# Kernel optimization log

Measured on AMD Instinct MI355X. Metric: run time of the kernel, lower is better.

Reference implementation:

```python
import jax, jax.numpy as jnp
import numpy as np

B, N, D, H = 2, 2048, 1024, 16
DH = D // H
MASK_VALUE = -1e7


def setup_inputs() -> dict:
    key = jax.random.key(0)
    ks = jax.random.split(key, 8)
    scale = 0.02
    return {
        "queries": jax.random.normal(ks[0], (B, N, D), dtype=jnp.float32),
        "keys": jax.random.normal(ks[1], (B, N, D), dtype=jnp.float32),
        "values": jax.random.normal(ks[2], (B, N, D), dtype=jnp.float32),
        "valid_len": jax.random.randint(ks[3], (B * H,), 1, N + 1, dtype=jnp.int32),
        "Wq": jax.random.normal(ks[4], (D, D), dtype=jnp.float32) * scale,
        "Wk": jax.random.normal(ks[5], (D, D), dtype=jnp.float32) * scale,
        "Wv": jax.random.normal(ks[6], (D, D), dtype=jnp.float32) * scale,
        "Wo": jax.random.normal(ks[7], (D, D), dtype=jnp.float32) * scale,
    }


def reference(queries, keys, values, valid_len, Wq, Wk, Wv, Wo):
    b, n, d = queries.shape
    h, dh = H, d // H

    def split_heads(x):  # (b, n, d) -> (b, h, n, dh)
        return x.reshape(b, n, h, dh).transpose(0, 2, 1, 3)

    q = split_heads(queries @ Wq)
    k = split_heads(keys @ Wk)
    v = split_heads(values @ Wv)

    # (b, h, nq, nk) full score tensor, as in the original naive bmm path
    scores = jnp.einsum("bhqd,bhkd->bhqk", q, k) / jnp.sqrt(jnp.float32(dh))

    # valid_len is 1-D of length b*h; repeat_interleave over queries means the
    # mask depends only on the key index: keep k < valid_len[bh]
    vl = valid_len.reshape(b, h, 1, 1)
    keep = jnp.arange(n)[None, None, None, :] < vl  # (b, h, 1, nk)
    scores = jnp.where(keep, scores, MASK_VALUE)

    attn = jax.nn.softmax(scores, axis=-1)
    heads = jnp.einsum("bhqk,bhkd->bhqd", attn, v)  # (b, h, n, dh)
    out = heads.transpose(0, 2, 1, 3).reshape(b, n, d) @ Wo
    return out
```

## Files before the change

### kernel.cpp

```cpp
#include <hip/hip_runtime.h>

#define B_ 2
#define N_ 2048
#define D_ 1024
#define H_ 16
#define DH_ 64
#define NITEMS 1024

typedef _Float16 half8 __attribute__((ext_vector_type(8)));
typedef _Float16 half4 __attribute__((ext_vector_type(4)));
typedef float f32x4 __attribute__((ext_vector_type(4)));

__device__ __forceinline__ void gl2lds16(const _Float16* g, _Float16* l) {
  __builtin_amdgcn_global_load_lds(
      (const __attribute__((address_space(1))) void*)g,
      (__attribute__((address_space(3))) void*)l, 16, 0, 0);
}

__global__ __launch_bounds__(256) void convert_x_kernel(
    const float* __restrict__ q, const float* __restrict__ k,
    const float* __restrict__ v, _Float16* __restrict__ dst) {
  const float* s = (blockIdx.y == 0) ? q : (blockIdx.y == 1) ? k : v;
  _Float16* d = dst + (size_t)blockIdx.y * ((size_t)B_ * N_ * D_);
  size_t idx = ((size_t)blockIdx.x * 256 + threadIdx.x) * 8;
  float4 a = *(const float4*)(s + idx);
  float4 b = *(const float4*)(s + idx + 4);
  half8 h;
  h[0] = (_Float16)a.x; h[1] = (_Float16)a.y; h[2] = (_Float16)a.z; h[3] = (_Float16)a.w;
  h[4] = (_Float16)b.x; h[5] = (_Float16)b.y; h[6] = (_Float16)b.z; h[7] = (_Float16)b.w;
  *(half8*)(d + idx) = h;
}

__global__ __launch_bounds__(256) void convert_w_kernel(
    const float* __restrict__ Wq, const float* __restrict__ Wk,
    const float* __restrict__ Wv, const float* __restrict__ Wo,
    _Float16* __restrict__ WtAll) {
  const float* W = (blockIdx.z == 0) ? Wq : (blockIdx.z == 1) ? Wk
                  : (blockIdx.z == 2) ? Wv : Wo;
  _Float16* Wt = WtAll + (size_t)blockIdx.z * D_ * D_;
  __shared__ float tile[64][65];
  int k0 = blockIdx.y * 64, n0 = blockIdx.x * 64;
  int tr = threadIdx.x >> 4, tc = threadIdx.x & 15;
#pragma unroll
  for (int i = 0; i < 4; ++i) {
    int r = tr + i * 16;
    float4 va = *(const float4*)(W + (size_t)(k0 + r) * D_ + n0 + tc * 4);
    tile[r][tc * 4 + 0] = va.x; tile[r][tc * 4 + 1] = va.y;
    tile[r][tc * 4 + 2] = va.z; tile[r][tc * 4 + 3] = va.w;
  }
  __syncthreads();
#pragma unroll
  for (int i = 0; i < 4; ++i) {
    int r = tr + i * 16;
    half4 hv;
    hv[0] = (_Float16)tile[tc * 4 + 0][r];
    hv[1] = (_Float16)tile[tc * 4 + 1][r];
    hv[2] = (_Float16)tile[tc * 4 + 2][r];
    hv[3] = (_Float16)tile[tc * 4 + 3][r];
    *(half4*)(Wt + (size_t)(n0 + r) * D_ + k0 + tc * 4) = hv;
  }
}

template <int NT, int MODE>
__global__ __launch_bounds__(256) void gemm_f16_kernel(
    const _Float16* __restrict__ Aall, const _Float16* __restrict__ Btall,
    _Float16* __restrict__ ChAll, float* __restrict__ Cf32) {
  constexpr int BN = NT * 32;
  constexpr int K = D_;
  __shared__ __attribute__((aligned(16))) _Float16 As[2][128 * 32];
  __shared__ __attribute__((aligned(16))) _Float16 Bs[2][BN * 32];
  const int z = blockIdx.z;
  const _Float16* A  = Aall  + (size_t)z * ((size_t)B_ * N_ * D_);
  const _Float16* Bt = Btall + (size_t)z * ((size_t)D_ * D_);
  _Float16* Chead = ChAll + (size_t)z * ((size_t)B_ * N_ * D_);

  const int tid = threadIdx.x;
  const int m0 = blockIdx.y * 128, n0 = blockIdx.x * BN;
  const int lane = tid & 63, w = tid >> 6;
  const int quad = lane >> 4, l15 = lane & 15;
  const int wm = (w >> 1) * 64, wn = (w & 1) * (BN / 2);
  const int sr = tid >> 2, sc4 = tid & 3;
  f32x4 acc[4][NT] = {};

  auto stage = [&](int kt, int buf) {
#pragma unroll
    for (int p = 0; p < 2; ++p) {
      int row = sr + p * 64;
      int gl = sc4 ^ ((row >> 1) & 3);
      gl2lds16(A + (size_t)(m0 + row) * K + kt + gl * 8,
               &As[buf][(row * 4 + sc4) * 8]);
    }
#pragma unroll
    for (int p = 0; p < NT / 2; ++p) {
      int row = sr + p * 64;
      int gl = sc4 ^ ((row >> 1) & 3);
      gl2lds16(Bt + (size_t)(n0 + row) * K + kt + gl * 8,
               &Bs[buf][(row * 4 + sc4) * 8]);
    }
  };

  stage(0, 0);
  __syncthreads();

  for (int kt = 0; kt < K / 32; ++kt) {
    const int cur = kt & 1;
    if (kt + 1 < K / 32) stage((kt + 1) * 32, 1 - cur);
    half8 af[4], bf[NT];
#pragma unroll
    for (int mt = 0; mt < 4; ++mt) {
      int row = wm + mt * 16 + l15;
      af[mt] = *(const half8*)&As[cur][(row * 4 + (quad ^ ((row >> 1) & 3))) * 8];
    }
#pragma unroll
    for (int nt = 0; nt < NT; ++nt) {
      int row = wn + nt * 16 + l15;
      bf[nt] = *(const half8*)&Bs[cur][(row * 4 + (quad ^ ((row >> 1) & 3))) * 8];
    }
#pragma unroll
    for (int mt = 0; mt < 4; ++mt)
#pragma unroll
      for (int nt = 0; nt < NT; ++nt)
        acc[mt][nt] = __builtin_amdgcn_mfma_f32_16x16x32_f16(
            af[mt], bf[nt], acc[mt][nt], 0, 0, 0);
    __syncthreads();
  }

#pragma unroll
  for (int mt = 0; mt < 4; ++mt) {
    int mrow = m0 + wm + mt * 16 + quad * 4;
#pragma unroll
    for (int nt = 0; nt < NT; ++nt) {
      int jcol = n0 + wn + nt * 16 + l15;
#pragma unroll
      for (int r = 0; r < 4; ++r) {
        float val = acc[mt][nt][r];
        int m = mrow + r;
        if (MODE == 0) {
          int b = m >> 11, n = m & (N_ - 1);
          int h = jcol >> 6, dh = jcol & (DH_ - 1);
          Chead[((((size_t)(b * H_ + h)) * N_ + n) * DH_) + dh] = (_Float16)val;
        } else {
          Cf32[(size_t)m * D_ + jcol] = val;
        }
      }
    }
  }
}

__global__ __launch_bounds__(256) void transpose_v_kernel(
    const _Float16* __restrict__ Vh, _Float16* __restrict__ VtG) {
  __shared__ float Ls[64][65];
  int bh = blockIdx.y, k0 = blockIdx.x * 64;
  int tid = threadIdx.x;
  const _Float16* src = Vh + (size_t)bh * N_ * DH_;
#pragma unroll
  for (int p = 0; p < 2; ++p) {
    int c = p * 256 + tid, row = c >> 3, pg = c & 7;
    half8 hv = *(const half8*)(src + (size_t)(k0 + row) * DH_ + pg * 8);
#pragma unroll
    for (int u = 0; u < 8; ++u) Ls[row][pg * 8 + u] = (float)hv[u];
  }
  __syncthreads();
  _Float16* dst = VtG + (size_t)bh * N_ * DH_;
#pragma unroll
  for (int p = 0; p < 2; ++p) {
    int c = p * 256 + tid, dh = c >> 3, pg = c & 7;
    half8 hv;
#pragma unroll
    for (int u = 0; u < 8; ++u) hv[u] = (_Float16)Ls[pg * 8 + u][dh];
    *(half8*)(dst + (size_t)dh * N_ + k0 + pg * 8) = hv;
  }
}

__global__ void sort_heads_kernel(const int* __restrict__ vlen,
                                  int* __restrict__ order) {
  int i = threadIdx.x;
  if (i < B_ * H_) {
    int vi = vlen[i], rank = 0;
    for (int j = 0; j < B_ * H_; ++j) {
      int vj = vlen[j];
      if (vj > vi || (vj == vi && j < i)) ++rank;
    }
    order[rank] = i;
  }
}

__global__ __launch_bounds__(256, 4) void attn_kernel(
    const _Float16* __restrict__ Qh, const _Float16* __restrict__ Kh,
    const _Float16* __restrict__ VtG, const int* __restrict__ vlen,
    _Float16* __restrict__ Hd, const int* __restrict__ order) {
  __shared__ __attribute__((aligned(16))) _Float16 Ks[2][64 * 64];
  __shared__ __attribute__((aligned(16))) _Float16 Vt[2][64 * 64];
  const int tid = threadIdx.x, lane = tid & 63, w = tid >> 6;
  const int quad = lane >> 4, l15 = lane & 15;
  const int sw  = (quad ^ (l15 & 7)) * 8;
  const int sw2 = ((quad + 4) ^ (l15 & 7)) * 8;
  const float sc2 = 0.125f * 1.44269504088896f;
  const half4 ones = {(_Float16)1, (_Float16)1, (_Float16)1, (_Float16)1};

#pragma unroll 1
  for (int half_ = 0; half_ < 2; ++half_) {
    const int item = half_ ? (NITEMS - 1 - (int)blockIdx.x) : (int)blockIdx.x;
    const int bh = order[item >> 5];
    const int q0 = (item & 31) * 64;
    const int b = bh >> 4, h = bh & (H_ - 1);
    const int vl = vlen[bh];
    const int KT = (vl + 63) >> 6;
    const _Float16* Qb = Qh  + (size_t)bh * N_ * DH_;
    const _Float16* Kb = Kh  + (size_t)bh * N_ * DH_;
    const _Float16* Vb = VtG + (size_t)bh * N_ * DH_;

    const half8 qb0 = *(const half8*)(Qb + (size_t)(q0 + w * 16 + l15) * DH_ + quad * 8);
    const half8 qb1 = *(const half8*)(Qb + (size_t)(q0 + w * 16 + l15) * DH_ + 32 + quad * 8);

    half8 kpre[2], vpre[2];
    auto prefetch = [&](int k0k) {
#pragma unroll
      for (int p = 0; p < 2; ++p) {
        int c = p * 256 + tid;
        int row = c >> 3, pg = c & 7;
        kpre[p] = *(const half8*)(Kb + (size_t)(k0k + row) * DH_ + (pg ^ (row & 7)) * 8);
        vpre[p] = *(const half8*)(Vb + (size_t)row * N_ + k0k + pg * 8);
      }
    };
    auto commit = [&](int buf) {
#pragma unroll
      for (int p = 0; p < 2; ++p) {
        int c = p * 256 + tid;
        int row = c >> 3, pg = c & 7;
        *(half8*)&Ks[buf][c * 8] = kpre[p];
        int j0 = (pg * 2) ^ (row & 15), j1 = (pg * 2 + 1) ^ (row & 15);
        half4 lo = {vpre[p][0], vpre[p][1], vpre[p][2], vpre[p][3]};
        half4 hi = {vpre[p][4], vpre[p][5], vpre[p][6], vpre[p][7]};
        *(half4*)&Vt[buf][row * 64 + j0 * 4] = lo;
        *(half4*)&Vt[buf][row * 64 + j1 * 4] = hi;
      }
    };

    if (half_) __syncthreads();
    prefetch(0);
    commit(0);
    if (KT > 1) prefetch(64);
    __syncthreads();

    f32x4 Oacc[4] = {};
    f32x4 lacc = {};

    for (int kt = 0; kt < KT; ++kt) {
      const int cur = kt & 1;
      if (kt + 1 < KT) commit(1 - cur);
      if (kt + 2 < KT) prefetch((kt + 2) * 64);

      f32x4 s[4];
#pragma unroll
      for (int nt = 0; nt < 4; ++nt) {
        int r = nt * 16 + l15;
        half8 ka0 = *(const half8*)&Ks[cur][r * 64 + sw];
        half8 ka1 = *(const half8*)&Ks[cur][r * 64 + sw2];
        f32x4 c = {};
        c = __builtin_amdgcn_mfma_f32_16x16x32_f16(ka0, qb0, c, 0, 0, 0);
        c = __builtin_amdgcn_mfma_f32_16x16x32_f16(ka1, qb1, c, 0, 0, 0);
        s[nt] = c;
      }
      const int k0k = kt * 64;
      half4 pf[4];
      if (k0k + 64 <= vl) {
#pragma unroll
        for (int nt = 0; nt < 4; ++nt)
#pragma unroll
          for (int r = 0; r < 4; ++r)
            pf[nt][r] = (_Float16)exp2f(s[nt][r] * sc2);
      } else {
#pragma unroll
        for (int nt = 0; nt < 4; ++nt) {
          int keyb = k0k + nt * 16 + quad * 4;
#pragma unroll
          for (int r = 0; r < 4; ++r) {
            float p = exp2f(s[nt][r] * sc2);
            pf[nt][r] = (keyb + r < vl) ? (_Float16)p : (_Float16)0.f;
          }
        }
      }
#pragma unroll
      for (int nt = 0; nt < 4; ++nt) {
        lacc = __builtin_amdgcn_mfma_f32_16x16x16f16(ones, pf[nt], lacc, 0, 0, 0);
#pragma unroll
        for (int dt = 0; dt < 4; ++dt) {
          int dh = dt * 16 + l15;
          half4 va = *(const half4*)&Vt[cur][dh * 64 + (((nt * 4 + quad) ^ l15) << 2)];
          Oacc[dt] = __builtin_amdgcn_mfma_f32_16x16x16f16(va, pf[nt], Oacc[dt], 0, 0, 0);
        }
      }
      __syncthreads();
    }

    float inv_l = 1.0f / lacc[0];
    int q = q0 + w * 16 + l15;
    _Float16* out = Hd + ((size_t)(b * N_ + q)) * D_ + h * DH_;
#pragma unroll
    for (int dt = 0; dt < 4; ++dt) {
      half4 o;
#pragma unroll
      for (int r = 0; r < 4; ++r) o[r] = (_Float16)(Oacc[dt][r] * inv_l);
      *(half4*)(out + dt * 16 + quad * 4) = o;
    }
  }
}

extern "C" void kernel_launch(void* const* d_in, const int* in_sizes, int n_in,
                              void* d_out, int out_size, void* d_ws, size_t ws_size,
                              hipStream_t stream) {
  const float* q  = (const float*)d_in[0];
  const float* k  = (const float*)d_in[1];
  const float* v  = (const float*)d_in[2];
  const int*   vl = (const int*)d_in[3];
  const float* Wq = (const float*)d_in[4];
  const float* Wk = (const float*)d_in[5];
  const float* Wv = (const float*)d_in[6];
  const float* Wo = (const float*)d_in[7];

  const size_t XSZ = (size_t)B_ * N_ * D_;
  const size_t WSZ = (size_t)D_ * D_;
  _Float16* ws = (_Float16*)d_ws;
  _Float16* Xf = ws;
  _Float16* Wt = Xf + 3 * XSZ;
  _Float16* Qh = Wt + 4 * WSZ;
  _Float16* Hd = Qh + 3 * XSZ;
  int* order = (int*)(Hd + XSZ);
  _Float16* VtG = Xf;

  convert_x_kernel<<<dim3(2048, 3), 256, 0, stream>>>(q, k, v, Xf);
  convert_w_kernel<<<dim3(16, 16, 4), 256, 0, stream>>>(Wq, Wk, Wv, Wo, Wt);

  gemm_f16_kernel<4, 0><<<dim3(D_ / 128, 32, 3), 256, 0, stream>>>(
      Xf, Wt, Qh, nullptr);

  transpose_v_kernel<<<dim3(N_ / 64, B_ * H_), 256, 0, stream>>>(
      Qh + 2 * XSZ, VtG);
  sort_heads_kernel<<<1, 64, 0, stream>>>(vl, order);

  attn_kernel<<<dim3(512), 256, 0, stream>>>(
      Qh, Qh + XSZ, VtG, vl, Hd, order);

  gemm_f16_kernel<2, 1><<<dim3(D_ / 64, 32, 1), 256, 0, stream>>>(
      Hd, Wt + 3 * WSZ, nullptr, (float*)d_out);
}
```

Measured before the change: 240.8 us.

## Merge prep kernels, single-buffer GEMM staging, one attention tile per block

Folds the X conversion, weight transpose-convert and head-sort kernels into one prep kernel launch, which removes two launches. The GEMM drops its double-buffered LDS staging for a single buffer with a sync before and after each k-step. This halves LDS use but stops loads from overlapping with MFMA work. The attention kernel now launches 1024 blocks, each handling one query tile, instead of 512 blocks that each paired a long and a short tile. Load balance across heads of different lengths now rests on the hardware scheduler and the sorted order.

```diff
diff --git a/kernel.cpp b/kernel.cpp
--- a/kernel.cpp
+++ b/kernel.cpp
@@ -17,49 +17,65 @@
       (__attribute__((address_space(3))) void*)l, 16, 0, 0);
 }
 
-__global__ __launch_bounds__(256) void convert_x_kernel(
+__global__ __launch_bounds__(256) void prep_kernel(
     const float* __restrict__ q, const float* __restrict__ k,
-    const float* __restrict__ v, _Float16* __restrict__ dst) {
-  const float* s = (blockIdx.y == 0) ? q : (blockIdx.y == 1) ? k : v;
-  _Float16* d = dst + (size_t)blockIdx.y * ((size_t)B_ * N_ * D_);
-  size_t idx = ((size_t)blockIdx.x * 256 + threadIdx.x) * 8;
-  float4 a = *(const float4*)(s + idx);
-  float4 b = *(const float4*)(s + idx + 4);
-  half8 h;
-  h[0] = (_Float16)a.x; h[1] = (_Float16)a.y; h[2] = (_Float16)a.z; h[3] = (_Float16)a.w;
-  h[4] = (_Float16)b.x; h[5] = (_Float16)b.y; h[6] = (_Float16)b.z; h[7] = (_Float16)b.w;
-  *(half8*)(d + idx) = h;
-}
-
-__global__ __launch_bounds__(256) void convert_w_kernel(
-    const float* __restrict__ Wq, const float* __restrict__ Wk,
-    const float* __restrict__ Wv, const float* __restrict__ Wo,
-    _Float16* __restrict__ WtAll) {
-  const float* W = (blockIdx.z == 0) ? Wq : (blockIdx.z == 1) ? Wk
-                  : (blockIdx.z == 2) ? Wv : Wo;
-  _Float16* Wt = WtAll + (size_t)blockIdx.z * D_ * D_;
+    const float* __restrict__ v, const float* __restrict__ Wq,
+    const float* __restrict__ Wk, const float* __restrict__ Wv,
+    const float* __restrict__ Wo, const int* __restrict__ vlen,
+    _Float16* __restrict__ Xf, _Float16* __restrict__ WtAll,
+    int* __restrict__ order) {
   __shared__ float tile[64][65];
-  int k0 = blockIdx.y * 64, n0 = blockIdx.x * 64;
-  int tr = threadIdx.x >> 4, tc = threadIdx.x & 15;
-#pragma unroll
-  for (int i = 0; i < 4; ++i) {
-    int r = tr + i * 16;
-    float4 va = *(const float4*)(W + (size_t)(k0 + r) * D_ + n0 + tc * 4);
-    tile[r][tc * 4 + 0] = va.x; tile[r][tc * 4 + 1] = va.y;
-    tile[r][tc * 4 + 2] = va.z; tile[r][tc * 4 + 3] = va.w;
-  }
-  __syncthreads();
-#pragma unroll
-  for (int i = 0; i < 4; ++i) {
-    int r = tr + i * 16;
-    half4 hv;
-    hv[0] = (_Float16)tile[tc * 4 + 0][r];
-    hv[1] = (_Float16)tile[tc * 4 + 1][r];
-    hv[2] = (_Float16)tile[tc * 4 + 2][r];
-    hv[3] = (_Float16)tile[tc * 4 + 3][r];
-    *(half4*)(Wt + (size_t)(n0 + r) * D_ + k0 + tc * 4) = hv;
-  }
-}
+  const int bid = blockIdx.x;
+  if (bid < 6144) {
+    int y = bid >> 11, x = bid & 2047;
+    const float* s = (y == 0) ? q : (y == 1) ? k : v;
+    _Float16* d = Xf + (size_t)y * ((size_t)B_ * N_ * D_);
+    size_t idx = ((size_t)x * 256 + threadIdx.x) * 8;
+    float4 a = *(const float4*)(s + idx);
+    float4 b = *(const float4*)(s + idx + 4);
+    half8 h;
+    h[0] = (_Float16)a.x; h[1] = (_Float16)a.y; h[2] = (_Float16)a.z; h[3] = (_Float16)a.w;
+    h[4] = (_Float16)b.x; h[5] = (_Float16)b.y; h[6] = (_Float16)b.z; h[7] = (_Float16)b.w;
+    *(half8*)(d + idx) = h;
+  } else if (bid < 6144 + 1024) {
+    int idx = bid - 6144;
+    int z = idx >> 8, rem = idx & 255, gy = rem >> 4, gx = rem & 15;
+    const float* W = (z == 0) ? Wq : (z == 1) ? Wk : (z == 2) ? Wv : Wo;
+    _Float16* Wt = WtAll + (size_t)z * D_ * D_;
+    int k0 = gy * 64, n0 = gx * 64;
+    int tr = threadIdx.x >> 4, tc = threadIdx.x & 15;
+#pragma unroll
+    for (int i = 0; i < 4; ++i) {
+      int r = tr + i * 16;
+      float4 va = *(const float4*)(W + (size_t)(k0 + r) * D_ + n0 + tc * 4);
+      tile[r][tc * 4 + 0] = va.x; tile[r][tc * 4 + 1] = va.y;
+      tile[r][tc * 4 + 2] = va.z; tile[r][tc * 4 + 3] = va.w;
+    }
+    __syncthreads();
+#pragma unroll
+    for (int i = 0; i < 4; ++i) {
+      int r = tr + i * 16;
+      half4 hv;
+      hv[0] = (_Float16)tile[tc * 4 + 0][r];
+      hv[1] = (_Float16)tile[tc * 4 + 1][r];
+      hv[2] = (_Float16)tile[tc * 4 + 2][r];
+      hv[3] = (_Float16)tile[tc * 4 + 3][r];
+      *(half4*)(Wt + (size_t)(n0 + r) * D_ + k0 + tc * 4) = hv;
+    }
+  } else {
+    int i = threadIdx.x;
+    if (i < B_ * H_) {
+      int vi = vlen[i], rank = 0;
+      for (int j = 0; j < B_ * H_; ++j) {
+        int vj = vlen[j];
+        if (vj > vi || (vj == vi && j < i)) ++rank;
+      }
+      order[rank] = i;
+    }
+  }
+}
+
+#define BK 32
 
 template <int NT, int MODE>
 __global__ __launch_bounds__(256) void gemm_f16_kernel(
@@ -67,8 +83,8 @@
     _Float16* __restrict__ ChAll, float* __restrict__ Cf32) {
   constexpr int BN = NT * 32;
   constexpr int K = D_;
-  __shared__ __attribute__((aligned(16))) _Float16 As[2][128 * 32];
-  __shared__ __attribute__((aligned(16))) _Float16 Bs[2][BN * 32];
+  __shared__ __attribute__((aligned(16))) _Float16 As[128 * BK];
+  __shared__ __attribute__((aligned(16))) _Float16 Bs[BN * BK];
   const int z = blockIdx.z;
   const _Float16* A  = Aall  + (size_t)z * ((size_t)B_ * N_ * D_);
   const _Float16* Bt = Btall + (size_t)z * ((size_t)D_ * D_);
@@ -79,50 +95,39 @@
   const int lane = tid & 63, w = tid >> 6;
   const int quad = lane >> 4, l15 = lane & 15;
   const int wm = (w >> 1) * 64, wn = (w & 1) * (BN / 2);
-  const int sr = tid >> 2, sc4 = tid & 3;
+  const int swz = (quad ^ ((l15 >> 1) & 3)) * 8;
   f32x4 acc[4][NT] = {};
 
-  auto stage = [&](int kt, int buf) {
+  for (int kt = 0; kt < K; kt += BK) {
+    if (kt) __syncthreads();
 #pragma unroll
     for (int p = 0; p < 2; ++p) {
-      int row = sr + p * 64;
-      int gl = sc4 ^ ((row >> 1) & 3);
-      gl2lds16(A + (size_t)(m0 + row) * K + kt + gl * 8,
-               &As[buf][(row * 4 + sc4) * 8]);
+      int c = p * 256 + tid;
+      int row = c >> 2, pg = c & 3;
+      int gl = pg ^ ((row >> 1) & 3);
+      gl2lds16(A + (size_t)(m0 + row) * K + kt + gl * 8, &As[c * 8]);
     }
 #pragma unroll
     for (int p = 0; p < NT / 2; ++p) {
-      int row = sr + p * 64;
-      int gl = sc4 ^ ((row >> 1) & 3);
-      gl2lds16(Bt + (size_t)(n0 + row) * K + kt + gl * 8,
-               &Bs[buf][(row * 4 + sc4) * 8]);
-    }
-  };
-
-  stage(0, 0);
-  __syncthreads();
-
-  for (int kt = 0; kt < K / 32; ++kt) {
-    const int cur = kt & 1;
-    if (kt + 1 < K / 32) stage((kt + 1) * 32, 1 - cur);
+      int c = p * 256 + tid;
+      int row = c >> 2, pg = c & 3;
+      int gl = pg ^ ((row >> 1) & 3);
+      gl2lds16(Bt + (size_t)(n0 + row) * K + kt + gl * 8, &Bs[c * 8]);
+    }
+    __syncthreads();
     half8 af[4], bf[NT];
 #pragma unroll
-    for (int mt = 0; mt < 4; ++mt) {
-      int row = wm + mt * 16 + l15;
-      af[mt] = *(const half8*)&As[cur][(row * 4 + (quad ^ ((row >> 1) & 3))) * 8];
-    }
-#pragma unroll
-    for (int nt = 0; nt < NT; ++nt) {
-      int row = wn + nt * 16 + l15;
-      bf[nt] = *(const half8*)&Bs[cur][(row * 4 + (quad ^ ((row >> 1) & 3))) * 8];
-    }
+    for (int mt = 0; mt < 4; ++mt)
+      af[mt] = *(const half8*)&As[(wm + mt * 16 + l15) * 32 + swz];
+#pragma unroll
+    for (int nt = 0; nt < NT; ++nt)
+      bf[nt] = *(const half8*)&Bs[(wn + nt * 16 + l15) * 32 + swz];
 #pragma unroll
     for (int mt = 0; mt < 4; ++mt)
 #pragma unroll
       for (int nt = 0; nt < NT; ++nt)
         acc[mt][nt] = __builtin_amdgcn_mfma_f32_16x16x32_f16(
             af[mt], bf[nt], acc[mt][nt], 0, 0, 0);
-    __syncthreads();
   }
 
 #pragma unroll
@@ -169,19 +174,6 @@
 #pragma unroll
     for (int u = 0; u < 8; ++u) hv[u] = (_Float16)Ls[pg * 8 + u][dh];
     *(half8*)(dst + (size_t)dh * N_ + k0 + pg * 8) = hv;
-  }
-}
-
-__global__ void sort_heads_kernel(const int* __restrict__ vlen,
-                                  int* __restrict__ order) {
-  int i = threadIdx.x;
-  if (i < B_ * H_) {
-    int vi = vlen[i], rank = 0;
-    for (int j = 0; j < B_ * H_; ++j) {
-      int vj = vlen[j];
-      if (vj > vi || (vj == vi && j < i)) ++rank;
-    }
-    order[rank] = i;
   }
 }
 
@@ -198,112 +190,108 @@
   const float sc2 = 0.125f * 1.44269504088896f;
   const half4 ones = {(_Float16)1, (_Float16)1, (_Float16)1, (_Float16)1};
 
-#pragma unroll 1
-  for (int half_ = 0; half_ < 2; ++half_) {
-    const int item = half_ ? (NITEMS - 1 - (int)blockIdx.x) : (int)blockIdx.x;
-    const int bh = order[item >> 5];
-    const int q0 = (item & 31) * 64;
-    const int b = bh >> 4, h = bh & (H_ - 1);
-    const int vl = vlen[bh];
-    const int KT = (vl + 63) >> 6;
-    const _Float16* Qb = Qh  + (size_t)bh * N_ * DH_;
-    const _Float16* Kb = Kh  + (size_t)bh * N_ * DH_;
-    const _Float16* Vb = VtG + (size_t)bh * N_ * DH_;
-
-    const half8 qb0 = *(const half8*)(Qb + (size_t)(q0 + w * 16 + l15) * DH_ + quad * 8);
-    const half8 qb1 = *(const half8*)(Qb + (size_t)(q0 + w * 16 + l15) * DH_ + 32 + quad * 8);
-
-    half8 kpre[2], vpre[2];
-    auto prefetch = [&](int k0k) {
-#pragma unroll
-      for (int p = 0; p < 2; ++p) {
-        int c = p * 256 + tid;
-        int row = c >> 3, pg = c & 7;
-        kpre[p] = *(const half8*)(Kb + (size_t)(k0k + row) * DH_ + (pg ^ (row & 7)) * 8);
-        vpre[p] = *(const half8*)(Vb + (size_t)row * N_ + k0k + pg * 8);
-      }
-    };
-    auto commit = [&](int buf) {
-#pragma unroll
-      for (int p = 0; p < 2; ++p) {
-        int c = p * 256 + tid;
-        int row = c >> 3, pg = c & 7;
-        *(half8*)&Ks[buf][c * 8] = kpre[p];
-        int j0 = (pg * 2) ^ (row & 15), j1 = (pg * 2 + 1) ^ (row & 15);
-        half4 lo = {vpre[p][0], vpre[p][1], vpre[p][2], vpre[p][3]};
-        half4 hi = {vpre[p][4], vpre[p][5], vpre[p][6], vpre[p][7]};
-        *(half4*)&Vt[buf][row * 64 + j0 * 4] = lo;
-        *(half4*)&Vt[buf][row * 64 + j1 * 4] = hi;
-      }
-    };
-
-    if (half_) __syncthreads();
-    prefetch(0);
-    commit(0);
-    if (KT > 1) prefetch(64);
-    __syncthreads();
-
-    f32x4 Oacc[4] = {};
-    f32x4 lacc = {};
-
-    for (int kt = 0; kt < KT; ++kt) {
-      const int cur = kt & 1;
-      if (kt + 1 < KT) commit(1 - cur);
-      if (kt + 2 < KT) prefetch((kt + 2) * 64);
-
-      f32x4 s[4];
+  const int item = blockIdx.x;
+  const int bh = order[item >> 5];
+  const int q0 = (item & 31) * 64;
+  const int b = bh >> 4, h = bh & (H_ - 1);
+  const int vl = vlen[bh];
+  const int KT = (vl + 63) >> 6;
+  const _Float16* Qb = Qh  + (size_t)bh * N_ * DH_;
+  const _Float16* Kb = Kh  + (size_t)bh * N_ * DH_;
+  const _Float16* Vb = VtG + (size_t)bh * N_ * DH_;
+
+  const half8 qb0 = *(const half8*)(Qb + (size_t)(q0 + w * 16 + l15) * DH_ + quad * 8);
+  const half8 qb1 = *(const half8*)(Qb + (size_t)(q0 + w * 16 + l15) * DH_ + 32 + quad * 8);
+
+  half8 kpre[2], vpre[2];
+  auto prefetch = [&](int k0k) {
+#pragma unroll
+    for (int p = 0; p < 2; ++p) {
+      int c = p * 256 + tid;
+      int row = c >> 3, pg = c & 7;
+      kpre[p] = *(const half8*)(Kb + (size_t)(k0k + row) * DH_ + (pg ^ (row & 7)) * 8);
+      vpre[p] = *(const half8*)(Vb + (size_t)row * N_ + k0k + pg * 8);
+    }
+  };
+  auto commit = [&](int buf) {
+#pragma unroll
+    for (int p = 0; p < 2; ++p) {
+      int c = p * 256 + tid;
+      int row = c >> 3, pg = c & 7;
+      *(half8*)&Ks[buf][c * 8] = kpre[p];
+      int j0 = (pg * 2) ^ (row & 15), j1 = (pg * 2 + 1) ^ (row & 15);
+      half4 lo = {vpre[p][0], vpre[p][1], vpre[p][2], vpre[p][3]};
+      half4 hi = {vpre[p][4], vpre[p][5], vpre[p][6], vpre[p][7]};
+      *(half4*)&Vt[buf][row * 64 + j0 * 4] = lo;
+      *(half4*)&Vt[buf][row * 64 + j1 * 4] = hi;
+    }
+  };
+
+  prefetch(0);
+  commit(0);
+  if (KT > 1) prefetch(64);
+  __syncthreads();
+
+  f32x4 Oacc[4] = {};
+  f32x4 lacc = {};
+
+  for (int kt = 0; kt < KT; ++kt) {
+    const int cur = kt & 1;
+    if (kt + 1 < KT) commit(1 - cur);
+    if (kt + 2 < KT) prefetch((kt + 2) * 64);
+
+    f32x4 s[4];
+#pragma unroll
+    for (int nt = 0; nt < 4; ++nt) {
+      int r = nt * 16 + l15;
+      half8 ka0 = *(const half8*)&Ks[cur][r * 64 + sw];
+      half8 ka1 = *(const half8*)&Ks[cur][r * 64 + sw2];
+      f32x4 c = {};
+      c = __builtin_amdgcn_mfma_f32_16x16x32_f16(ka0, qb0, c, 0, 0, 0);
+      c = __builtin_amdgcn_mfma_f32_16x16x32_f16(ka1, qb1, c, 0, 0, 0);
+      s[nt] = c;
+    }
+    const int k0k = kt * 64;
+    half4 pf[4];
+    if (k0k + 64 <= vl) {
+#pragma unroll
+      for (int nt = 0; nt < 4; ++nt)
+#pragma unroll
+        for (int r = 0; r < 4; ++r)
+          pf[nt][r] = (_Float16)exp2f(s[nt][r] * sc2);
+    } else {
 #pragma unroll
       for (int nt = 0; nt < 4; ++nt) {
-        int r = nt * 16 + l15;
-        half8 ka0 = *(const half8*)&Ks[cur][r * 64 + sw];
-        half8 ka1 = *(const half8*)&Ks[cur][r * 64 + sw2];
-        f32x4 c = {};
-        c = __builtin_amdgcn_mfma_f32_16x16x32_f16(ka0, qb0, c, 0, 0, 0);
-        c = __builtin_amdgcn_mfma_f32_16x16x32_f16(ka1, qb1, c, 0, 0, 0);
-        s[nt] = c;
-      }
-      const int k0k = kt * 64;
-      half4 pf[4];
-      if (k0k + 64 <= vl) {
-#pragma unroll
-        for (int nt = 0; nt < 4; ++nt)
-#pragma unroll
-          for (int r = 0; r < 4; ++r)
-            pf[nt][r] = (_Float16)exp2f(s[nt][r] * sc2);
-      } else {
-#pragma unroll
-        for (int nt = 0; nt < 4; ++nt) {
-          int keyb = k0k + nt * 16 + quad * 4;
-#pragma unroll
-          for (int r = 0; r < 4; ++r) {
-            float p = exp2f(s[nt][r] * sc2);
-            pf[nt][r] = (keyb + r < vl) ? (_Float16)p : (_Float16)0.f;
-          }
+        int keyb = k0k + nt * 16 + quad * 4;
+#pragma unroll
+        for (int r = 0; r < 4; ++r) {
+          float p = exp2f(s[nt][r] * sc2);
+          pf[nt][r] = (keyb + r < vl) ? (_Float16)p : (_Float16)0.f;
         }
       }
-#pragma unroll
-      for (int nt = 0; nt < 4; ++nt) {
-        lacc = __builtin_amdgcn_mfma_f32_16x16x16f16(ones, pf[nt], lacc, 0, 0, 0);
-#pragma unroll
-        for (int dt = 0; dt < 4; ++dt) {
-          int dh = dt * 16 + l15;
-          half4 va = *(const half4*)&Vt[cur][dh * 64 + (((nt * 4 + quad) ^ l15) << 2)];
-          Oacc[dt] = __builtin_amdgcn_mfma_f32_16x16x16f16(va, pf[nt], Oacc[dt], 0, 0, 0);
-        }
+    }
+#pragma unroll
+    for (int nt = 0; nt < 4; ++nt) {
+      lacc = __builtin_amdgcn_mfma_f32_16x16x16f16(ones, pf[nt], lacc, 0, 0, 0);
+#pragma unroll
+      for (int dt = 0; dt < 4; ++dt) {
+        int dh = dt * 16 + l15;
+        half4 va = *(const half4*)&Vt[cur][dh * 64 + (((nt * 4 + quad) ^ l15) << 2)];
+        Oacc[dt] = __builtin_amdgcn_mfma_f32_16x16x16f16(va, pf[nt], Oacc[dt], 0, 0, 0);
       }
-      __syncthreads();
-    }
-
-    float inv_l = 1.0f / lacc[0];
-    int q = q0 + w * 16 + l15;
-    _Float16* out = Hd + ((size_t)(b * N_ + q)) * D_ + h * DH_;
-#pragma unroll
-    for (int dt = 0; dt < 4; ++dt) {
-      half4 o;
-#pragma unroll
-      for (int r = 0; r < 4; ++r) o[r] = (_Float16)(Oacc[dt][r] * inv_l);
-      *(half4*)(out + dt * 16 + quad * 4) = o;
-    }
+    }
+    __syncthreads();
+  }
+
+  float inv_l = 1.0f / lacc[0];
+  int q = q0 + w * 16 + l15;
+  _Float16* out = Hd + ((size_t)(b * N_ + q)) * D_ + h * DH_;
+#pragma unroll
+  for (int dt = 0; dt < 4; ++dt) {
+    half4 o;
+#pragma unroll
+    for (int r = 0; r < 4; ++r) o[r] = (_Float16)(Oacc[dt][r] * inv_l);
+    *(half4*)(out + dt * 16 + quad * 4) = o;
   }
 }
 
@@ -329,17 +317,16 @@
   int* order = (int*)(Hd + XSZ);
   _Float16* VtG = Xf;
 
-  convert_x_kernel<<<dim3(2048, 3), 256, 0, stream>>>(q, k, v, Xf);
-  convert_w_kernel<<<dim3(16, 16, 4), 256, 0, stream>>>(Wq, Wk, Wv, Wo, Wt);
+  prep_kernel<<<dim3(6144 + 1024 + 1), 256, 0, stream>>>(
+      q, k, v, Wq, Wk, Wv, Wo, vl, Xf, Wt, order);
 
   gemm_f16_kernel<4, 0><<<dim3(D_ / 128, 32, 3), 256, 0, stream>>>(
       Xf, Wt, Qh, nullptr);
 
   transpose_v_kernel<<<dim3(N_ / 64, B_ * H_), 256, 0, stream>>>(
       Qh + 2 * XSZ, VtG);
-  sort_heads_kernel<<<1, 64, 0, stream>>>(vl, order);
-
-  attn_kernel<<<dim3(512), 256, 0, stream>>>(
+
+  attn_kernel<<<dim3(NITEMS), 256, 0, stream>>>(
       Qh, Qh + XSZ, VtG, vl, Hd, order);
 
   gemm_f16_kernel<2, 1><<<dim3(D_ / 64, 32, 1), 256, 0, stream>>>(
```

Result: faster. 222.6 us (-7.6%).
